# Performance work log

Measured on AMD Instinct MI355X. Metric: run time of the kernel, lower is better.

The kernel has to match this reference:

```python
import jax, jax.numpy as jnp
import numpy as np

N, E = 50000, 800000
IN_DIM, EDGE_DIM, HID, OUT_DIM, L = 128, 16, 64, 8, 4
MSG_EPS = 1e-7  # GENConv eps added to relu(msg)


def layer_norm(x, g, b, eps=1e-5):
    mu = x.mean(-1, keepdims=True)
    var = ((x - mu) ** 2).mean(-1, keepdims=True)
    return (x - mu) * jax.lax.rsqrt(var + eps) * g + b


def segment_softmax(logits, seg, num_segments):
    # numerically stable softmax over edges grouped by destination node
    m = jax.ops.segment_max(logits, seg, num_segments=num_segments)
    m = jnp.where(jnp.isfinite(m), m, 0.0)
    e = jnp.exp(logits - m[seg])
    s = jax.ops.segment_sum(e, seg, num_segments=num_segments)
    return e / (s[seg] + 1e-16)


def gen_conv(x, src, dst, ea, t, W1, b1, g1, be1, W2, b2):
    # GENConv: message = relu(x_j + e_ij) + eps, softmax-aggregate by dst, add root, MLP [h->2h->h]
    msg = jax.nn.relu(x[src] + ea) + MSG_EPS          # [E, H]
    alpha = segment_softmax(msg * t, dst, x.shape[0]) # [E, H]
    agg = jax.ops.segment_sum(msg * alpha, dst, num_segments=x.shape[0])  # [N, H]
    h = agg + x
    h = jax.nn.relu(layer_norm(h @ W1 + b1, g1, be1))  # [N, 2H]
    return h @ W2 + b2                                 # [N, H]


def setup_inputs() -> dict:
    key = jax.random.key(0)
    ks = jax.random.split(key, 16)
    sc = 0.05
    inp = {
        "x": jax.random.normal(ks[0], (N, IN_DIM), jnp.float32),
        "edge_attr": jax.random.normal(ks[1], (E, EDGE_DIM), jnp.float32),
        "node_W": jax.random.normal(ks[2], (IN_DIM, HID), jnp.float32) * sc,
        "node_b": jnp.zeros((HID,), jnp.float32),
        "edge_W": jax.random.normal(ks[3], (EDGE_DIM, HID), jnp.float32) * sc,
        "edge_b": jnp.zeros((HID,), jnp.float32),
        "conv_t": jnp.ones((L,), jnp.float32),
        "conv_W1": jax.random.normal(ks[4], (L, HID, 2 * HID), jnp.float32) * sc,
        "conv_b1": jnp.zeros((L, 2 * HID), jnp.float32),
        "conv_g1": jnp.ones((L, 2 * HID), jnp.float32),
        "conv_be1": jnp.zeros((L, 2 * HID), jnp.float32),
        "conv_W2": jax.random.normal(ks[5], (L, 2 * HID, HID), jnp.float32) * sc,
        "conv_b2": jnp.zeros((L, HID), jnp.float32),
        "ln_g": jnp.ones((L, HID), jnp.float32),
        "ln_b": jnp.zeros((L, HID), jnp.float32),
        "lin_W": jax.random.normal(ks[6], (HID, OUT_DIM), jnp.float32) * sc,
        "lin_b": jnp.zeros((OUT_DIM,), jnp.float32),
        "edge_index": jax.random.randint(ks[7], (2, E), 0, N, jnp.int64),
    }
    return inp


def reference(x, edge_attr, node_W, node_b, edge_W, edge_b,
              conv_t, conv_W1, conv_b1, conv_g1, conv_be1, conv_W2, conv_b2,
              ln_g, ln_b, lin_W, lin_b, edge_index):
    src, dst = edge_index[0], edge_index[1]  # flow: source_to_target
    h = x @ node_W + node_b
    ea = edge_attr @ edge_W + edge_b
    # first layer: conv only (DeeperGCN applies layers[0].conv directly)
    h = gen_conv(h, src, dst, ea, conv_t[0], conv_W1[0], conv_b1[0],
                 conv_g1[0], conv_be1[0], conv_W2[0], conv_b2[0])
    # res+ blocks: x + conv(dropout(relu(norm(x)))); dropout inactive (eval)
    for i in range(1, L):
        z = jax.nn.relu(layer_norm(h, ln_g[i], ln_b[i]))
        h = h + gen_conv(z, src, dst, ea, conv_t[i], conv_W1[i], conv_b1[i],
                         conv_g1[i], conv_be1[i], conv_W2[i], conv_b2[i])
    h = jax.nn.relu(layer_norm(h, ln_g[0], ln_b[0]))
    return h @ lin_W + lin_b
```

## Files before the change

### kernel.cpp

```cpp
#include <hip/hip_runtime.h>
#include <hip/hip_fp16.h>

#define N_NODES 50000
#define N_EDGES 800000
#define IN_DIM  128
#define EDGE_DIM 16
#define HID     64
#define HID2    128
#define OUT_DIM 8
#define N_LAYERS 4
#define NBUCK   391
#define CCHUNK  4096
#define CBLOCKS 196

typedef _Float16 half8 __attribute__((ext_vector_type(8)));
typedef float floatx4 __attribute__((ext_vector_type(4)));

static __device__ __forceinline__ float bcast(float v, int l) {
    return __uint_as_float(__builtin_amdgcn_readlane(__float_as_uint(v), l));
}

__global__ __launch_bounds__(256, 4) void chist_kernel(
    const int* __restrict__ dsts, int* __restrict__ ccnt)
{
    __shared__ int lh[NBUCK];
    for (int i = threadIdx.x; i < NBUCK; i += 256) lh[i] = 0;
    __syncthreads();
    const int base = blockIdx.x * CCHUNK;
#pragma unroll
    for (int i = 0; i < 16; ++i) {
        const int e = base + i * 256 + threadIdx.x;
        if (e < N_EDGES) atomicAdd(&lh[dsts[e] >> 7], 1);
    }
    __syncthreads();
    for (int i = threadIdx.x; i < NBUCK; i += 256)
        if (lh[i]) atomicAdd(&ccnt[i], lh[i]);
}

__global__ __launch_bounds__(256, 1) void cscan_kernel(
    const int* __restrict__ ccnt, int* __restrict__ coff, int* __restrict__ ccur)
{
    __shared__ int part[512];
    const int t = threadIdx.x;
    part[t]       = (t < NBUCK)       ? ccnt[t]       : 0;
    part[t + 256] = (t + 256 < NBUCK) ? ccnt[t + 256] : 0;
    __syncthreads();
    for (int off = 1; off < 512; off <<= 1) {
        const int v0 = (t >= off) ? part[t - off] : 0;
        const int v1 = (t + 256 >= off) ? part[t + 256 - off] : 0;
        __syncthreads();
        part[t] += v0; part[t + 256] += v1;
        __syncthreads();
    }
    if (t < NBUCK) { const int ex = (t > 0) ? part[t - 1] : 0; coff[t] = ex; ccur[t] = ex; }
    const int i2 = t + 256;
    if (i2 < NBUCK) { coff[i2] = part[i2 - 1]; ccur[i2] = part[i2 - 1]; }
    if (t == 0) coff[NBUCK] = part[NBUCK - 1];
}

__global__ __launch_bounds__(256, 4) void cscatter_kernel(
    const int* __restrict__ srcs, const int* __restrict__ dsts,
    int* __restrict__ ccur, uint2* __restrict__ tmp)
{
    __shared__ int lh[NBUCK], lbase[NBUCK], lrank[NBUCK];
    for (int i = threadIdx.x; i < NBUCK; i += 256) { lh[i] = 0; lrank[i] = 0; }
    __syncthreads();
    const int base = blockIdx.x * CCHUNK;
    int myd[16], mys[16];
#pragma unroll
    for (int i = 0; i < 16; ++i) {
        const int e = base + i * 256 + threadIdx.x;
        if (e < N_EDGES) {
            myd[i] = dsts[e]; mys[i] = srcs[e];
            atomicAdd(&lh[myd[i] >> 7], 1);
        } else myd[i] = -1;
    }
    __syncthreads();
    for (int i = threadIdx.x; i < NBUCK; i += 256) {
        const int c = lh[i];
        lbase[i] = c ? atomicAdd(&ccur[i], c) : 0;
    }
    __syncthreads();
#pragma unroll
    for (int i = 0; i < 16; ++i) {
        if (myd[i] >= 0) {
            const int e = base + i * 256 + threadIdx.x;
            const int b = myd[i] >> 7;
            const int r = atomicAdd(&lrank[b], 1);
            tmp[lbase[b] + r] =
                make_uint2((unsigned)mys[i] | ((unsigned)myd[i] << 16),
                           (unsigned)e);
        }
    }
}

__global__ __launch_bounds__(256, 1) void fsort_kernel(
    const uint2* __restrict__ tmp, const int* __restrict__ coff,
    unsigned* __restrict__ sd2, int* __restrict__ eid)
{
    __shared__ uint2 ebuf[4096];
    __shared__ int lh[128], lsc[128];
    const int b = blockIdx.x;
    const int lo = coff[b];
    const int cnt = coff[b + 1] - lo;
    if (threadIdx.x < 128) lh[threadIdx.x] = 0;
    __syncthreads();
    for (int i = threadIdx.x; i < cnt; i += 256) {
        const uint2 v = tmp[lo + i];
        ebuf[i] = v;
        atomicAdd(&lh[(int)(v.x >> 16) - b * 128], 1);
    }
    __syncthreads();
    if (threadIdx.x < 128) lsc[threadIdx.x] = lh[threadIdx.x];
    __syncthreads();
    for (int off = 1; off < 128; off <<= 1) {
        int v = 0;
        if (threadIdx.x < 128 && threadIdx.x >= off) v = lsc[threadIdx.x - off];
        __syncthreads();
        if (threadIdx.x < 128) lsc[threadIdx.x] += v;
        __syncthreads();
    }
    if (threadIdx.x < 128) lh[threadIdx.x] = lsc[threadIdx.x] - lh[threadIdx.x];
    __syncthreads();
    for (int i = threadIdx.x; i < cnt; i += 256) {
        const uint2 v = ebuf[i];
        const int d = (int)(v.x >> 16) - b * 128;
        const int pos = atomicAdd(&lh[d], 1);
        sd2[lo + pos] = v.x;
        eid[lo + pos] = (int)v.y;
    }
}

__global__ __launch_bounds__(256, 2) void node_proj_kernel(
    const float* __restrict__ x, const float* __restrict__ W,
    const float* __restrict__ b, float* __restrict__ h, __half* __restrict__ zh)
{
    __shared__ float xs[4][IN_DIM];
    const int c = threadIdx.x & 63;
    const int local_n = threadIdx.x >> 6;
    float w[IN_DIM];
#pragma unroll
    for (int k = 0; k < IN_DIM; ++k) w[k] = W[k * HID + c];
    const float bias = b[c];

    for (int base = blockIdx.x * 4; base < N_NODES; base += gridDim.x * 4) {
        __syncthreads();
#pragma unroll
        for (int i = 0; i < 2; ++i) {
            int idx = threadIdx.x + i * 256;
            int nn = idx >> 7, kk = idx & 127;
            xs[nn][kk] = x[(base + nn) * IN_DIM + kk];
        }
        __syncthreads();
        const int n = base + local_n;
        float acc = bias;
#pragma unroll
        for (int k4 = 0; k4 < IN_DIM / 4; ++k4) {
            float4 xv = ((const float4*)xs[local_n])[k4];
            acc = fmaf(xv.x, w[k4 * 4 + 0], acc);
            acc = fmaf(xv.y, w[k4 * 4 + 1], acc);
            acc = fmaf(xv.z, w[k4 * 4 + 2], acc);
            acc = fmaf(xv.w, w[k4 * 4 + 3], acc);
        }
        h[n * HID + c] = acc;
        zh[n * HID + c] = __float2half(acc);
    }
}

__global__ __launch_bounds__(256, 4) void edge_emb_kernel(
    const float* __restrict__ ea, const float* __restrict__ W,
    const float* __restrict__ b, const int* __restrict__ eid,
    __half* __restrict__ eah)
{
    __shared__ __half lds_t[4][16 * HID];
    const int lane = threadIdx.x & 63;
    const int waveid = threadIdx.x >> 6;
    const int wave = (blockIdx.x * 256 + threadIdx.x) >> 6;
    const int nwaves = gridDim.x * 4;
    const int m = lane & 15, q = lane >> 4;
    const int NT = N_EDGES / 16;

    half8 bf[4];
#pragma unroll
    for (int blk = 0; blk < 4; ++blk) {
#pragma unroll
        for (int i = 0; i < 8; ++i) {
            const int k = q * 8 + i;
            bf[blk][i] = (k < EDGE_DIM)
                ? (_Float16)W[k * HID + blk * 16 + m] : (_Float16)0.f;
        }
    }
    float bv[4];
#pragma unroll
    for (int blk = 0; blk < 4; ++blk) bv[blk] = b[blk * 16 + m];

    const int ed = lane >> 3, ch = lane & 7;

    for (int tile = wave; tile < NT; tile += nwaves) {
        const int e0 = tile * 16;
        const int eidx = eid[e0 + m];
        half8 af;
#pragma unroll
        for (int i = 0; i < 8; ++i) af[i] = (_Float16)0.f;
        if (q < 2) {
            const float4* ap =
                (const float4*)(ea + (size_t)eidx * EDGE_DIM + q * 8);
            const float4 lo = ap[0];
            const float4 hi = ap[1];
            af[0] = (_Float16)lo.x; af[1] = (_Float16)lo.y;
            af[2] = (_Float16)lo.z; af[3] = (_Float16)lo.w;
            af[4] = (_Float16)hi.x; af[5] = (_Float16)hi.y;
            af[6] = (_Float16)hi.z; af[7] = (_Float16)hi.w;
        }
        floatx4 c[4];
#pragma unroll
        for (int blk = 0; blk < 4; ++blk) {
            floatx4 cin = {bv[blk], bv[blk], bv[blk], bv[blk]};
            c[blk] = __builtin_amdgcn_mfma_f32_16x16x32_f16(
                af, bf[blk], cin, 0, 0, 0);
        }
#pragma unroll
        for (int blk = 0; blk < 4; ++blk)
#pragma unroll
            for (int r = 0; r < 4; ++r)
                lds_t[waveid][(q * 4 + r) * HID + blk * 16 + m] =
                    __float2half(c[blk][r]);
        const float4 v0 =
            *(const float4*)&lds_t[waveid][ed * HID + ch * 8];
        const float4 v1 =
            *(const float4*)&lds_t[waveid][(8 + ed) * HID + ch * 8];
        ((float4*)(eah + (size_t)(e0 + ed) * HID))[ch] = v0;
        ((float4*)(eah + (size_t)(e0 + 8 + ed) * HID))[ch] = v1;
    }
}

__global__ __launch_bounds__(256, 4) void edge_agg_kernel(
    const __half* __restrict__ zh, const __half* __restrict__ eah,
    const unsigned* __restrict__ sd2,
    const float* __restrict__ conv_t, int layer,
    float* __restrict__ p, float* __restrict__ s)
{
    const int lane = threadIdx.x & 63;
    const int wave = (blockIdx.x * 256 + threadIdx.x) >> 6;
    const int nwaves = gridDim.x * 4;
    const float t2 = conv_t[layer] * 1.4426950408889634f;
    const int NT = N_EDGES / 64;

    const _Float16* zf = (const _Float16*)zh;
    const _Float16* ef = (const _Float16*)eah;

    for (int tile = wave; tile < NT; tile += nwaves) {
        const int e0 = tile * 64;
        const unsigned sdv = sd2[e0 + lane];
        const int sv = (int)(sdv & 0xffffu);
        const int dv = (int)(sdv >> 16);
        const int pv = __shfl_up(dv, 1, 64);
        const unsigned long long bmask = __ballot(dv != pv) & ~1ull;
        const _Float16* erow = ef + (size_t)e0 * HID + lane;

        _Float16 za[8], ez[8], zb[8], eb[8];
#pragma unroll
        for (int k = 0; k < 8; ++k) {
            const int a = __builtin_amdgcn_readlane(sv, k);
            za[k] = (zf + (size_t)a * HID)[lane];
            ez[k] = erow[(size_t)k * HID];
        }

        float S = 0.f, P = 0.f;
        int cur = __builtin_amdgcn_readlane(dv, 0);
#pragma unroll
        for (int g = 0; g < 8; ++g) {
            if (g < 7) {
#pragma unroll
                for (int k = 0; k < 8; ++k) {
                    const int a = __builtin_amdgcn_readlane(sv, (g + 1) * 8 + k);
                    zb[k] = (zf + (size_t)a * HID)[lane];
                    eb[k] = erow[(size_t)((g + 1) * 8 + k) * HID];
                }
            }
#pragma unroll
            for (int k = 0; k < 8; ++k) {
                const int j = g * 8 + k;
                if (bmask & (1ull << j)) {
                    unsafeAtomicAdd(&s[(size_t)cur * HID + lane], S);
                    unsafeAtomicAdd(&p[(size_t)cur * HID + lane], P);
                    S = 0.f; P = 0.f;
                    cur = __builtin_amdgcn_readlane(dv, j);
                }
                _Float16 mh = za[k] + ez[k];
                mh = mh > (_Float16)0.f ? mh : (_Float16)0.f;
                const float m = (float)mh + 1e-7f;
                const float xx = __builtin_amdgcn_exp2f(m * t2);
                S += xx;
                P = fmaf(m, xx, P);
            }
            if (g < 7) {
#pragma unroll
                for (int k = 0; k < 8; ++k) { za[k] = zb[k]; ez[k] = eb[k]; }
            }
        }
        unsafeAtomicAdd(&s[(size_t)cur * HID + lane], S);
        unsafeAtomicAdd(&p[(size_t)cur * HID + lane], P);
    }
}

__global__ __launch_bounds__(256, 3) void node_mm1_kernel(
    float* __restrict__ p, float* __restrict__ s,
    const __half* __restrict__ zh,
    const float* __restrict__ W1, const float* __restrict__ b1,
    const float* __restrict__ g1, const float* __restrict__ be1,
    __half* __restrict__ vh)
{
    const int lane = threadIdx.x & 63;
    const int wave = (blockIdx.x * 256 + threadIdx.x) >> 6;
    const int nwaves = gridDim.x * 4;

    float wa[HID], wb[HID];
#pragma unroll
    for (int k = 0; k < HID; ++k) {
        wa[k] = W1[k * HID2 + lane];
        wb[k] = W1[k * HID2 + 64 + lane];
    }
    const float ba = b1[lane],  bb = b1[64 + lane];
    const float ga = g1[lane],  gb = g1[64 + lane];
    const float ca = be1[lane], cb = be1[64 + lane];

    for (int n = wave; n < N_NODES; n += nwaves) {
        const int idx = n * HID + lane;
        const float pv = p[idx];
        const float sv = s[idx];
        const float zv = __half2float(zh[idx]);
        p[idx] = 0.f;
        s[idx] = 0.f;
        const float hv = pv / (sv + 1e-16f) + zv;

        float a0 = 0.f, a1 = 0.f, c0 = 0.f, c1 = 0.f;
#pragma unroll
        for (int k = 0; k < 32; ++k) {
            const float x0 = bcast(hv, k);
            const float x1 = bcast(hv, k + 32);
            a0 = fmaf(x0, wa[k], a0);
            c0 = fmaf(x0, wb[k], c0);
            a1 = fmaf(x1, wa[k + 32], a1);
            c1 = fmaf(x1, wb[k + 32], c1);
        }
        const float ua = (a0 + a1) + ba;
        const float ub = (c0 + c1) + bb;

        float sum = ua + ub;
#pragma unroll
        for (int o = 1; o < 64; o <<= 1) sum += __shfl_xor(sum, o, 64);
        const float mu = sum * (1.f / 128.f);
        const float da = ua - mu, db = ub - mu;
        float q = fmaf(da, da, db * db);
#pragma unroll
        for (int o = 1; o < 64; o <<= 1) q += __shfl_xor(q, o, 64);
        const float rstd = rsqrtf(q * (1.f / 128.f) + 1e-5f);
        const float ya = da * rstd * ga + ca;
        const float yb = db * rstd * gb + cb;
        vh[(size_t)n * HID2 + lane]      = __float2half(ya > 0.f ? ya : 0.f);
        vh[(size_t)n * HID2 + 64 + lane] = __float2half(yb > 0.f ? yb : 0.f);
    }
}

__global__ __launch_bounds__(256, 3) void node_mm2_kernel(
    const __half* __restrict__ vh,
    const float* __restrict__ W2, const float* __restrict__ b2,
    const float* __restrict__ lng, const float* __restrict__ lnb,
    float* __restrict__ h, __half* __restrict__ zh, int residual)
{
    const int lane = threadIdx.x & 63;
    const int wave = (blockIdx.x * 256 + threadIdx.x) >> 6;
    const int nwaves = gridDim.x * 4;

    float wa[HID2 / 2], wb[HID2 / 2];
#pragma unroll
    for (int k = 0; k < HID2 / 2; ++k) {
        wa[k] = W2[k * HID + lane];
        wb[k] = W2[(k + 64) * HID + lane];
    }
    const float bias = b2[lane];
    const float g = lng[lane];
    const float be = lnb[lane];

    for (int n = wave; n < N_NODES; n += nwaves) {
        const float f0 = __half2float(vh[(size_t)n * HID2 + lane]);
        const float f1 = __half2float(vh[(size_t)n * HID2 + 64 + lane]);

        float a0 = 0.f, a1 = 0.f, c0 = 0.f, c1 = 0.f;
#pragma unroll
        for (int k = 0; k < 32; ++k) {
            const float x0 = bcast(f0, k);
            const float x1 = bcast(f0, k + 32);
            const float x2 = bcast(f1, k);
            const float x3 = bcast(f1, k + 32);
            a0 = fmaf(x0, wa[k], a0);
            a1 = fmaf(x1, wa[k + 32], a1);
            c0 = fmaf(x2, wb[k], c0);
            c1 = fmaf(x3, wb[k + 32], c1);
        }
        const float acc = (a0 + a1) + (c0 + c1) + bias;

        const int idx = n * HID + lane;
        const float hn = residual ? (h[idx] + acc) : acc;
        h[idx] = hn;

        float sum = hn;
#pragma unroll
        for (int o = 1; o < 64; o <<= 1) sum += __shfl_xor(sum, o, 64);
        const float mu = sum * (1.f / 64.f);
        const float d = hn - mu;
        float q = d * d;
#pragma unroll
        for (int o = 1; o < 64; o <<= 1) q += __shfl_xor(q, o, 64);
        const float var = q * (1.f / 64.f);
        const float y = d * rsqrtf(var + 1e-5f) * g + be;
        zh[idx] = __float2half(y > 0.f ? y : 0.f);
    }
}

__global__ __launch_bounds__(256, 4) void final_kernel(
    const __half* __restrict__ zh, const float* __restrict__ Wl,
    const float* __restrict__ bl, float* __restrict__ out)
{
    __shared__ float wl[HID * OUT_DIM];
    for (int i = threadIdx.x; i < HID * OUT_DIM; i += 256) wl[i] = Wl[i];
    __syncthreads();
    const int total = N_NODES * OUT_DIM;
    for (int idx = blockIdx.x * 256 + threadIdx.x; idx < total;
         idx += gridDim.x * 256) {
        const int n = idx >> 3, o = idx & 7;
        const __half2* zp = (const __half2*)(zh + (size_t)n * HID);
        float acc = bl[o];
#pragma unroll
        for (int k2 = 0; k2 < HID / 2; ++k2) {
            const float2 f = __half22float2(zp[k2]);
            acc = fmaf(f.x, wl[(k2 * 2 + 0) * OUT_DIM + o], acc);
            acc = fmaf(f.y, wl[(k2 * 2 + 1) * OUT_DIM + o], acc);
        }
        out[idx] = acc;
    }
}

extern "C" void kernel_launch(void* const* d_in, const int* in_sizes, int n_in,
                              void* d_out, int out_size, void* d_ws, size_t ws_size,
                              hipStream_t stream)
{
    const float* x         = (const float*)d_in[0];
    const float* edge_attr = (const float*)d_in[1];
    const float* node_W    = (const float*)d_in[2];
    const float* node_b    = (const float*)d_in[3];
    const float* edge_W    = (const float*)d_in[4];
    const float* edge_b    = (const float*)d_in[5];
    const float* conv_t    = (const float*)d_in[6];
    const float* conv_W1   = (const float*)d_in[7];
    const float* conv_b1   = (const float*)d_in[8];
    const float* conv_g1   = (const float*)d_in[9];
    const float* conv_be1  = (const float*)d_in[10];
    const float* conv_W2   = (const float*)d_in[11];
    const float* conv_b2   = (const float*)d_in[12];
    const float* ln_g      = (const float*)d_in[13];
    const float* ln_b      = (const float*)d_in[14];
    const float* lin_W     = (const float*)d_in[15];
    const float* lin_b     = (const float*)d_in[16];
    const int*   edge_index= (const int*)d_in[17];
    const int*   srcs = edge_index;
    const int*   dsts = edge_index + N_EDGES;
    float* out = (float*)d_out;

    float* h   = (float*)d_ws;
    float* p   = h   + N_NODES * HID;
    float* s   = p   + N_NODES * HID;
    __half* vh  = (__half*)(s + N_NODES * HID);
    __half* zh  = vh + (size_t)N_NODES * HID2;
    __half* eah = zh + (size_t)N_NODES * HID;
    uint2* tmp  = (uint2*)(eah + (size_t)N_EDGES * HID);
    unsigned* sd2 = (unsigned*)(tmp + N_EDGES);
    int* eid    = (int*)(sd2 + N_EDGES);
    int* ccnt   = eid + N_EDGES;
    int* coff   = ccnt + NBUCK;
    int* ccur   = coff + NBUCK + 1;

    hipMemsetAsync(ccnt, 0, (size_t)NBUCK * sizeof(int), stream);
    chist_kernel<<<CBLOCKS, 256, 0, stream>>>(dsts, ccnt);
    cscan_kernel<<<1, 256, 0, stream>>>(ccnt, coff, ccur);
    cscatter_kernel<<<CBLOCKS, 256, 0, stream>>>(srcs, dsts, ccur, tmp);
    fsort_kernel<<<NBUCK, 256, 0, stream>>>(tmp, coff, sd2, eid);

    node_proj_kernel<<<2048, 256, 0, stream>>>(x, node_W, node_b, h, zh);
    edge_emb_kernel<<<3125, 256, 0, stream>>>(edge_attr, edge_W, edge_b, eid, eah);

    hipMemsetAsync(p, 0, (size_t)2 * N_NODES * HID * sizeof(float), stream);

    for (int layer = 0; layer < N_LAYERS; ++layer) {
        edge_agg_kernel<<<3125, 256, 0, stream>>>(zh, eah, sd2,
                                                  conv_t, layer, p, s);
        node_mm1_kernel<<<2048, 256, 0, stream>>>(
            p, s, zh,
            conv_W1 + (size_t)layer * HID * HID2, conv_b1 + layer * HID2,
            conv_g1 + layer * HID2, conv_be1 + layer * HID2, vh);
        const float* gz = (layer < N_LAYERS - 1) ? (ln_g + (layer + 1) * HID) : ln_g;
        const float* bz = (layer < N_LAYERS - 1) ? (ln_b + (layer + 1) * HID) : ln_b;
        node_mm2_kernel<<<2048, 256, 0, stream>>>(
            vh, conv_W2 + (size_t)layer * HID2 * HID, conv_b2 + layer * HID,
            gz, bz, h, zh, layer > 0 ? 1 : 0);
    }
    final_kernel<<<1024, 256, 0, stream>>>(zh, lin_W, lin_b, out);
}
```

Before: 670.4 us.

## Fuse edge embedding projection into per-layer edge aggregation kernel

Removes the precomputed fp16 edge-embedding buffer and instead recomputes the edge_attr projection with MFMA inside each layer's aggregation kernel, staging results through a rotated LDS buffer for per-lane access. This trades reading a large materialised edge-feature array four times for gathering the smaller raw edge attributes and doing redundant matrix work per layer. It raises LDS usage and register pressure and may reduce occupancy.

```diff
diff --git a/kernel.cpp b/kernel.cpp
--- a/kernel.cpp
+++ b/kernel.cpp
@@ -14,6 +14,7 @@
 #define CBLOCKS 196
 
 typedef _Float16 half8 __attribute__((ext_vector_type(8)));
+typedef _Float16 half2f __attribute__((ext_vector_type(2)));
 typedef float floatx4 __attribute__((ext_vector_type(4)));
 
 static __device__ __forceinline__ float bcast(float v, int l) {
@@ -167,18 +168,23 @@
     }
 }
 
-__global__ __launch_bounds__(256, 4) void edge_emb_kernel(
-    const float* __restrict__ ea, const float* __restrict__ W,
-    const float* __restrict__ b, const int* __restrict__ eid,
-    __half* __restrict__ eah)
-{
-    __shared__ __half lds_t[4][16 * HID];
+__global__ __launch_bounds__(256, 4) void edge_agg_kernel(
+    const __half* __restrict__ zh,
+    const float* __restrict__ ea, const float* __restrict__ eW,
+    const float* __restrict__ eb_, const int* __restrict__ eid,
+    const unsigned* __restrict__ sd2,
+    const float* __restrict__ conv_t, int layer,
+    float* __restrict__ p, float* __restrict__ s)
+{
+    __shared__ _Float16 lbuf[4][64 * 64];
     const int lane = threadIdx.x & 63;
     const int waveid = threadIdx.x >> 6;
     const int wave = (blockIdx.x * 256 + threadIdx.x) >> 6;
     const int nwaves = gridDim.x * 4;
+    const float t2 = conv_t[layer] * 1.4426950408889634f;
+    const int NT = N_EDGES / 64;
     const int m = lane & 15, q = lane >> 4;
-    const int NT = N_EDGES / 16;
+    const int rot = m * 4;
 
     half8 bf[4];
 #pragma unroll
@@ -187,67 +193,15 @@
         for (int i = 0; i < 8; ++i) {
             const int k = q * 8 + i;
             bf[blk][i] = (k < EDGE_DIM)
-                ? (_Float16)W[k * HID + blk * 16 + m] : (_Float16)0.f;
+                ? (_Float16)eW[k * HID + blk * 16 + m] : (_Float16)0.f;
         }
     }
     float bv[4];
 #pragma unroll
-    for (int blk = 0; blk < 4; ++blk) bv[blk] = b[blk * 16 + m];
-
-    const int ed = lane >> 3, ch = lane & 7;
-
-    for (int tile = wave; tile < NT; tile += nwaves) {
-        const int e0 = tile * 16;
-        const int eidx = eid[e0 + m];
-        half8 af;
-#pragma unroll
-        for (int i = 0; i < 8; ++i) af[i] = (_Float16)0.f;
-        if (q < 2) {
-            const float4* ap =
-                (const float4*)(ea + (size_t)eidx * EDGE_DIM + q * 8);
-            const float4 lo = ap[0];
-            const float4 hi = ap[1];
-            af[0] = (_Float16)lo.x; af[1] = (_Float16)lo.y;
-            af[2] = (_Float16)lo.z; af[3] = (_Float16)lo.w;
-            af[4] = (_Float16)hi.x; af[5] = (_Float16)hi.y;
-            af[6] = (_Float16)hi.z; af[7] = (_Float16)hi.w;
-        }
-        floatx4 c[4];
-#pragma unroll
-        for (int blk = 0; blk < 4; ++blk) {
-            floatx4 cin = {bv[blk], bv[blk], bv[blk], bv[blk]};
-            c[blk] = __builtin_amdgcn_mfma_f32_16x16x32_f16(
-                af, bf[blk], cin, 0, 0, 0);
-        }
-#pragma unroll
-        for (int blk = 0; blk < 4; ++blk)
-#pragma unroll
-            for (int r = 0; r < 4; ++r)
-                lds_t[waveid][(q * 4 + r) * HID + blk * 16 + m] =
-                    __float2half(c[blk][r]);
-        const float4 v0 =
-            *(const float4*)&lds_t[waveid][ed * HID + ch * 8];
-        const float4 v1 =
-            *(const float4*)&lds_t[waveid][(8 + ed) * HID + ch * 8];
-        ((float4*)(eah + (size_t)(e0 + ed) * HID))[ch] = v0;
-        ((float4*)(eah + (size_t)(e0 + 8 + ed) * HID))[ch] = v1;
-    }
-}
-
-__global__ __launch_bounds__(256, 4) void edge_agg_kernel(
-    const __half* __restrict__ zh, const __half* __restrict__ eah,
-    const unsigned* __restrict__ sd2,
-    const float* __restrict__ conv_t, int layer,
-    float* __restrict__ p, float* __restrict__ s)
-{
-    const int lane = threadIdx.x & 63;
-    const int wave = (blockIdx.x * 256 + threadIdx.x) >> 6;
-    const int nwaves = gridDim.x * 4;
-    const float t2 = conv_t[layer] * 1.4426950408889634f;
-    const int NT = N_EDGES / 64;
+    for (int blk = 0; blk < 4; ++blk) bv[blk] = eb_[blk * 16 + m];
 
     const _Float16* zf = (const _Float16*)zh;
-    const _Float16* ef = (const _Float16*)eah;
+    _Float16* lrow = &lbuf[waveid][lane * 64];
 
     for (int tile = wave; tile < NT; tile += nwaves) {
         const int e0 = tile * 64;
@@ -256,14 +210,52 @@
         const int dv = (int)(sdv >> 16);
         const int pv = __shfl_up(dv, 1, 64);
         const unsigned long long bmask = __ballot(dv != pv) & ~1ull;
-        const _Float16* erow = ef + (size_t)e0 * HID + lane;
+
+        half8 afv[4];
+#pragma unroll
+        for (int t = 0; t < 4; ++t) {
+            const int eidx = eid[e0 + t * 16 + m];
+#pragma unroll
+            for (int i = 0; i < 8; ++i) afv[t][i] = (_Float16)0.f;
+            if (q < 2) {
+                const float4* ap =
+                    (const float4*)(ea + (size_t)eidx * EDGE_DIM + q * 8);
+                const float4 lo = ap[0];
+                const float4 hi = ap[1];
+                afv[t][0] = (_Float16)lo.x; afv[t][1] = (_Float16)lo.y;
+                afv[t][2] = (_Float16)lo.z; afv[t][3] = (_Float16)lo.w;
+                afv[t][4] = (_Float16)hi.x; afv[t][5] = (_Float16)hi.y;
+                afv[t][6] = (_Float16)hi.z; afv[t][7] = (_Float16)hi.w;
+            }
+        }
+#pragma unroll
+        for (int t = 0; t < 4; ++t) {
+#pragma unroll
+            for (int blk = 0; blk < 4; ++blk) {
+                floatx4 cin = {bv[blk], bv[blk], bv[blk], bv[blk]};
+                const floatx4 cc = __builtin_amdgcn_mfma_f32_16x16x32_f16(
+                    afv[t], bf[blk], cin, 0, 0, 0);
+                const int feat = blk * 16 + m;
+                const int col = (t * 16 + q * 4 + rot) & 63;
+                half2f h01, h23;
+                h01[0] = (_Float16)cc[0]; h01[1] = (_Float16)cc[1];
+                h23[0] = (_Float16)cc[2]; h23[1] = (_Float16)cc[3];
+                *(half2f*)&lbuf[waveid][feat * 64 + col]     = h01;
+                *(half2f*)&lbuf[waveid][feat * 64 + col + 2] = h23;
+            }
+        }
 
         _Float16 za[8], ez[8], zb[8], eb[8];
 #pragma unroll
         for (int k = 0; k < 8; ++k) {
             const int a = __builtin_amdgcn_readlane(sv, k);
             za[k] = (zf + (size_t)a * HID)[lane];
-            ez[k] = erow[(size_t)k * HID];
+        }
+#pragma unroll
+        for (int k2 = 0; k2 < 4; ++k2) {
+            const int col = (k2 * 2 + rot) & 63;
+            const half2f v = *(const half2f*)&lrow[col];
+            ez[2 * k2] = v[0]; ez[2 * k2 + 1] = v[1];
         }
 
         float S = 0.f, P = 0.f;
@@ -275,7 +267,12 @@
                 for (int k = 0; k < 8; ++k) {
                     const int a = __builtin_amdgcn_readlane(sv, (g + 1) * 8 + k);
                     zb[k] = (zf + (size_t)a * HID)[lane];
-                    eb[k] = erow[(size_t)((g + 1) * 8 + k) * HID];
+                }
+#pragma unroll
+                for (int k2 = 0; k2 < 4; ++k2) {
+                    const int col = ((g + 1) * 8 + k2 * 2 + rot) & 63;
+                    const half2f v = *(const half2f*)&lrow[col];
+                    eb[2 * k2] = v[0]; eb[2 * k2 + 1] = v[1];
                 }
             }
 #pragma unroll
@@ -289,10 +286,10 @@
                 }
                 _Float16 mh = za[k] + ez[k];
                 mh = mh > (_Float16)0.f ? mh : (_Float16)0.f;
-                const float m = (float)mh + 1e-7f;
-                const float xx = __builtin_amdgcn_exp2f(m * t2);
+                const float mm = (float)mh + 1e-7f;
+                const float xx = __builtin_amdgcn_exp2f(mm * t2);
                 S += xx;
-                P = fmaf(m, xx, P);
+                P = fmaf(mm, xx, P);
             }
             if (g < 7) {
 #pragma unroll
@@ -473,8 +470,7 @@
     float* s   = p   + N_NODES * HID;
     __half* vh  = (__half*)(s + N_NODES * HID);
     __half* zh  = vh + (size_t)N_NODES * HID2;
-    __half* eah = zh + (size_t)N_NODES * HID;
-    uint2* tmp  = (uint2*)(eah + (size_t)N_EDGES * HID);
+    uint2* tmp  = (uint2*)(zh + (size_t)N_NODES * HID);
     unsigned* sd2 = (unsigned*)(tmp + N_EDGES);
     int* eid    = (int*)(sd2 + N_EDGES);
     int* ccnt   = eid + N_EDGES;
@@ -488,13 +484,12 @@
     fsort_kernel<<<NBUCK, 256, 0, stream>>>(tmp, coff, sd2, eid);
 
     node_proj_kernel<<<2048, 256, 0, stream>>>(x, node_W, node_b, h, zh);
-    edge_emb_kernel<<<3125, 256, 0, stream>>>(edge_attr, edge_W, edge_b, eid, eah);
 
     hipMemsetAsync(p, 0, (size_t)2 * N_NODES * HID * sizeof(float), stream);
 
     for (int layer = 0; layer < N_LAYERS; ++layer) {
-        edge_agg_kernel<<<3125, 256, 0, stream>>>(zh, eah, sd2,
-                                                  conv_t, layer, p, s);
+        edge_agg_kernel<<<3125, 256, 0, stream>>>(
+            zh, edge_attr, edge_W, edge_b, eid, sd2, conv_t, layer, p, s);
         node_mm1_kernel<<<2048, 256, 0, stream>>>(
             p, s, zh,
             conv_W1 + (size_t)layer * HID * HID2, conv_b1 + layer * HID2,
```

After: 748.4 us. 11.6% more time.

## Switch edge aggregation to CSR per-node waves, removing atomics and memsets

Applied to the files above, without the earlier changes.

The sort kernel now also writes per-node row offsets (CSR) over the dst-sorted edge list. Edge aggregation assigns one wave per destination node and walks its incoming edges with a 4-deep prefetch. It writes P and S directly instead of using atomic adds, which also removes the zero-fill memset and the clearing stores in node_mm1. The risk is load imbalance from variable node degree (about 16 on average), which leaves many partially used 64-edge batches and shorter memory-level parallelism per wave than the old 64-edge tiles.

```diff
diff --git a/kernel.cpp b/kernel.cpp
--- a/kernel.cpp
+++ b/kernel.cpp
@@ -96,7 +96,8 @@
 
 __global__ __launch_bounds__(256, 1) void fsort_kernel(
     const uint2* __restrict__ tmp, const int* __restrict__ coff,
-    unsigned* __restrict__ sd2, int* __restrict__ eid)
+    unsigned* __restrict__ sd2, int* __restrict__ eid,
+    int* __restrict__ roff)
 {
     __shared__ uint2 ebuf[4096];
     __shared__ int lh[128], lsc[128];
@@ -120,7 +121,12 @@
         if (threadIdx.x < 128) lsc[threadIdx.x] += v;
         __syncthreads();
     }
-    if (threadIdx.x < 128) lh[threadIdx.x] = lsc[threadIdx.x] - lh[threadIdx.x];
+    if (threadIdx.x < 128) {
+        lh[threadIdx.x] = lsc[threadIdx.x] - lh[threadIdx.x];
+        roff[b * 128 + threadIdx.x] = lo + lh[threadIdx.x];
+        if (b == NBUCK - 1 && threadIdx.x == 127)
+            roff[NBUCK * 128] = lo + cnt;
+    }
     __syncthreads();
     for (int i = threadIdx.x; i < cnt; i += 256) {
         const uint2 v = ebuf[i];
@@ -236,7 +242,7 @@
 
 __global__ __launch_bounds__(256, 4) void edge_agg_kernel(
     const __half* __restrict__ zh, const __half* __restrict__ eah,
-    const unsigned* __restrict__ sd2,
+    const unsigned* __restrict__ sd2, const int* __restrict__ roff,
     const float* __restrict__ conv_t, int layer,
     float* __restrict__ p, float* __restrict__ s)
 {
@@ -244,68 +250,67 @@
     const int wave = (blockIdx.x * 256 + threadIdx.x) >> 6;
     const int nwaves = gridDim.x * 4;
     const float t2 = conv_t[layer] * 1.4426950408889634f;
-    const int NT = N_EDGES / 64;
+    const float et2 = 1e-7f * t2;
 
     const _Float16* zf = (const _Float16*)zh;
     const _Float16* ef = (const _Float16*)eah;
 
-    for (int tile = wave; tile < NT; tile += nwaves) {
-        const int e0 = tile * 64;
-        const unsigned sdv = sd2[e0 + lane];
-        const int sv = (int)(sdv & 0xffffu);
-        const int dv = (int)(sdv >> 16);
-        const int pv = __shfl_up(dv, 1, 64);
-        const unsigned long long bmask = __ballot(dv != pv) & ~1ull;
-        const _Float16* erow = ef + (size_t)e0 * HID + lane;
-
-        _Float16 za[8], ez[8], zb[8], eb[8];
-#pragma unroll
-        for (int k = 0; k < 8; ++k) {
-            const int a = __builtin_amdgcn_readlane(sv, k);
-            za[k] = (zf + (size_t)a * HID)[lane];
-            ez[k] = erow[(size_t)k * HID];
-        }
-
+    for (int n = wave; n < N_NODES; n += nwaves) {
+        const int lo = roff[n];
+        const int d = roff[n + 1] - lo;
         float S = 0.f, P = 0.f;
-        int cur = __builtin_amdgcn_readlane(dv, 0);
-#pragma unroll
-        for (int g = 0; g < 8; ++g) {
-            if (g < 7) {
-#pragma unroll
-                for (int k = 0; k < 8; ++k) {
-                    const int a = __builtin_amdgcn_readlane(sv, (g + 1) * 8 + k);
-                    zb[k] = (zf + (size_t)a * HID)[lane];
-                    eb[k] = erow[(size_t)((g + 1) * 8 + k) * HID];
+
+        for (int base = 0; base < d; base += 64) {
+            const int cnt = (d - base < 64) ? (d - base) : 64;
+            const unsigned sdv = sd2[lo + base + (lane < cnt ? lane : cnt - 1)];
+            const _Float16* ep = ef + (size_t)(lo + base) * HID + lane;
+
+            _Float16 zr[4], er[4];
+#pragma unroll
+            for (int k = 0; k < 4; ++k) {
+                if (k < cnt) {
+                    const int a = (int)(__builtin_amdgcn_readlane(sdv, k) & 0xffffu);
+                    zr[k] = zf[(size_t)a * HID + lane];
+                    er[k] = ep[(size_t)k * HID];
                 }
             }
-#pragma unroll
-            for (int k = 0; k < 8; ++k) {
-                const int j = g * 8 + k;
-                if (bmask & (1ull << j)) {
-                    unsafeAtomicAdd(&s[(size_t)cur * HID + lane], S);
-                    unsafeAtomicAdd(&p[(size_t)cur * HID + lane], P);
-                    S = 0.f; P = 0.f;
-                    cur = __builtin_amdgcn_readlane(dv, j);
+            int i = 0;
+            for (; i + 4 <= cnt; i += 4) {
+#pragma unroll
+                for (int k = 0; k < 4; ++k) {
+                    _Float16 mh = zr[k] + er[k];
+                    mh = mh > (_Float16)0.f ? mh : (_Float16)0.f;
+                    const float mm = (float)mh;
+                    const float xx = __builtin_amdgcn_exp2f(fmaf(mm, t2, et2));
+                    S += xx;
+                    P = fmaf(mm + 1e-7f, xx, P);
+                    const int nx = i + 4 + k;
+                    if (nx < cnt) {
+                        const int a = (int)(__builtin_amdgcn_readlane(sdv, nx) & 0xffffu);
+                        zr[k] = zf[(size_t)a * HID + lane];
+                        er[k] = ep[(size_t)nx * HID];
+                    }
                 }
-                _Float16 mh = za[k] + ez[k];
-                mh = mh > (_Float16)0.f ? mh : (_Float16)0.f;
-                const float m = (float)mh + 1e-7f;
-                const float xx = __builtin_amdgcn_exp2f(m * t2);
-                S += xx;
-                P = fmaf(m, xx, P);
             }
-            if (g < 7) {
-#pragma unroll
-                for (int k = 0; k < 8; ++k) { za[k] = zb[k]; ez[k] = eb[k]; }
+#pragma unroll
+            for (int k = 0; k < 4; ++k) {
+                if (i + k < cnt) {
+                    _Float16 mh = zr[k] + er[k];
+                    mh = mh > (_Float16)0.f ? mh : (_Float16)0.f;
+                    const float mm = (float)mh;
+                    const float xx = __builtin_amdgcn_exp2f(fmaf(mm, t2, et2));
+                    S += xx;
+                    P = fmaf(mm + 1e-7f, xx, P);
+                }
             }
         }
-        unsafeAtomicAdd(&s[(size_t)cur * HID + lane], S);
-        unsafeAtomicAdd(&p[(size_t)cur * HID + lane], P);
+        p[(size_t)n * HID + lane] = P;
+        s[(size_t)n * HID + lane] = S;
     }
 }
 
 __global__ __launch_bounds__(256, 3) void node_mm1_kernel(
-    float* __restrict__ p, float* __restrict__ s,
+    const float* __restrict__ p, const float* __restrict__ s,
     const __half* __restrict__ zh,
     const float* __restrict__ W1, const float* __restrict__ b1,
     const float* __restrict__ g1, const float* __restrict__ be1,
@@ -330,8 +335,6 @@
         const float pv = p[idx];
         const float sv = s[idx];
         const float zv = __half2float(zh[idx]);
-        p[idx] = 0.f;
-        s[idx] = 0.f;
         const float hv = pv / (sv + 1e-16f) + zv;
 
         float a0 = 0.f, a1 = 0.f, c0 = 0.f, c1 = 0.f;
@@ -477,7 +480,8 @@
     uint2* tmp  = (uint2*)(eah + (size_t)N_EDGES * HID);
     unsigned* sd2 = (unsigned*)(tmp + N_EDGES);
     int* eid    = (int*)(sd2 + N_EDGES);
-    int* ccnt   = eid + N_EDGES;
+    int* roff   = eid + N_EDGES;
+    int* ccnt   = roff + NBUCK * 128 + 1;
     int* coff   = ccnt + NBUCK;
     int* ccur   = coff + NBUCK + 1;
 
@@ -485,15 +489,13 @@
     chist_kernel<<<CBLOCKS, 256, 0, stream>>>(dsts, ccnt);
     cscan_kernel<<<1, 256, 0, stream>>>(ccnt, coff, ccur);
     cscatter_kernel<<<CBLOCKS, 256, 0, stream>>>(srcs, dsts, ccur, tmp);
-    fsort_kernel<<<NBUCK, 256, 0, stream>>>(tmp, coff, sd2, eid);
+    fsort_kernel<<<NBUCK, 256, 0, stream>>>(tmp, coff, sd2, eid, roff);
 
     node_proj_kernel<<<2048, 256, 0, stream>>>(x, node_W, node_b, h, zh);
     edge_emb_kernel<<<3125, 256, 0, stream>>>(edge_attr, edge_W, edge_b, eid, eah);
 
-    hipMemsetAsync(p, 0, (size_t)2 * N_NODES * HID * sizeof(float), stream);
-
     for (int layer = 0; layer < N_LAYERS; ++layer) {
-        edge_agg_kernel<<<3125, 256, 0, stream>>>(zh, eah, sd2,
+        edge_agg_kernel<<<6250, 256, 0, stream>>>(zh, eah, sd2, roff,
                                                   conv_t, layer, p, s);
         node_mm1_kernel<<<2048, 256, 0, stream>>>(
             p, s, zh,
```

After: 781.8 us. 16.6% more time.

## Fuse node MLP kernels and deepen edge aggregation prefetch

Applied to the files above, without the earlier changes.

Merges the two node MLP kernels into one that splits each node's 128-wide hidden layer across two waves and combines partial results through shared memory. This removes the intermediate fp16 hidden buffer and one launch per layer. The edge aggregation kernel now loads all 64 edge embeddings up front and gathers source features 16 at a time, with occupancy lowered to 3 blocks per SM to fit the extra registers. The fused kernel adds block-level barriers per node pair.

```diff
diff --git a/kernel.cpp b/kernel.cpp
--- a/kernel.cpp
+++ b/kernel.cpp
@@ -234,7 +234,7 @@
     }
 }
 
-__global__ __launch_bounds__(256, 4) void edge_agg_kernel(
+__global__ __launch_bounds__(256, 3) void edge_agg_kernel(
     const __half* __restrict__ zh, const __half* __restrict__ eah,
     const unsigned* __restrict__ sd2,
     const float* __restrict__ conv_t, int layer,
@@ -252,51 +252,54 @@
     for (int tile = wave; tile < NT; tile += nwaves) {
         const int e0 = tile * 64;
         const unsigned sdv = sd2[e0 + lane];
+        const _Float16* erow = ef + (size_t)e0 * HID + lane;
+
+        _Float16 ez[64];
+#pragma unroll
+        for (int k = 0; k < 64; ++k) ez[k] = erow[(size_t)k * HID];
+
         const int sv = (int)(sdv & 0xffffu);
         const int dv = (int)(sdv >> 16);
         const int pv = __shfl_up(dv, 1, 64);
         const unsigned long long bmask = __ballot(dv != pv) & ~1ull;
-        const _Float16* erow = ef + (size_t)e0 * HID + lane;
-
-        _Float16 za[8], ez[8], zb[8], eb[8];
-#pragma unroll
-        for (int k = 0; k < 8; ++k) {
+
+        _Float16 za[16], zb[16];
+#pragma unroll
+        for (int k = 0; k < 16; ++k) {
             const int a = __builtin_amdgcn_readlane(sv, k);
-            za[k] = (zf + (size_t)a * HID)[lane];
-            ez[k] = erow[(size_t)k * HID];
+            za[k] = zf[(size_t)a * HID + lane];
         }
 
         float S = 0.f, P = 0.f;
         int cur = __builtin_amdgcn_readlane(dv, 0);
 #pragma unroll
-        for (int g = 0; g < 8; ++g) {
-            if (g < 7) {
-#pragma unroll
-                for (int k = 0; k < 8; ++k) {
-                    const int a = __builtin_amdgcn_readlane(sv, (g + 1) * 8 + k);
-                    zb[k] = (zf + (size_t)a * HID)[lane];
-                    eb[k] = erow[(size_t)((g + 1) * 8 + k) * HID];
+        for (int g = 0; g < 4; ++g) {
+            if (g < 3) {
+#pragma unroll
+                for (int k = 0; k < 16; ++k) {
+                    const int a = __builtin_amdgcn_readlane(sv, (g + 1) * 16 + k);
+                    zb[k] = zf[(size_t)a * HID + lane];
                 }
             }
 #pragma unroll
-            for (int k = 0; k < 8; ++k) {
-                const int j = g * 8 + k;
+            for (int k = 0; k < 16; ++k) {
+                const int j = g * 16 + k;
                 if (bmask & (1ull << j)) {
                     unsafeAtomicAdd(&s[(size_t)cur * HID + lane], S);
                     unsafeAtomicAdd(&p[(size_t)cur * HID + lane], P);
                     S = 0.f; P = 0.f;
                     cur = __builtin_amdgcn_readlane(dv, j);
                 }
-                _Float16 mh = za[k] + ez[k];
+                _Float16 mh = za[k] + ez[j];
                 mh = mh > (_Float16)0.f ? mh : (_Float16)0.f;
-                const float m = (float)mh + 1e-7f;
-                const float xx = __builtin_amdgcn_exp2f(m * t2);
+                const float mm = (float)mh + 1e-7f;
+                const float xx = __builtin_amdgcn_exp2f(mm * t2);
                 S += xx;
-                P = fmaf(m, xx, P);
+                P = fmaf(mm, xx, P);
             }
-            if (g < 7) {
-#pragma unroll
-                for (int k = 0; k < 8; ++k) { za[k] = zb[k]; ez[k] = eb[k]; }
+            if (g < 3) {
+#pragma unroll
+                for (int k = 0; k < 16; ++k) za[k] = zb[k];
             }
         }
         unsafeAtomicAdd(&s[(size_t)cur * HID + lane], S);
@@ -304,118 +307,88 @@
     }
 }
 
-__global__ __launch_bounds__(256, 3) void node_mm1_kernel(
+__global__ __launch_bounds__(256, 3) void node_mlp_kernel(
     float* __restrict__ p, float* __restrict__ s,
-    const __half* __restrict__ zh,
     const float* __restrict__ W1, const float* __restrict__ b1,
     const float* __restrict__ g1, const float* __restrict__ be1,
-    __half* __restrict__ vh)
-{
+    const float* __restrict__ W2, const float* __restrict__ b2,
+    const float* __restrict__ lng, const float* __restrict__ lnb,
+    float* __restrict__ h, __half* zh, int residual)
+{
+    __shared__ float part1[2][HID];
+    __shared__ float red[2][2][2];
     const int lane = threadIdx.x & 63;
-    const int wave = (blockIdx.x * 256 + threadIdx.x) >> 6;
-    const int nwaves = gridDim.x * 4;
-
-    float wa[HID], wb[HID];
-#pragma unroll
-    for (int k = 0; k < HID; ++k) {
-        wa[k] = W1[k * HID2 + lane];
-        wb[k] = W1[k * HID2 + 64 + lane];
-    }
-    const float ba = b1[lane],  bb = b1[64 + lane];
-    const float ga = g1[lane],  gb = g1[64 + lane];
-    const float ca = be1[lane], cb = be1[64 + lane];
-
-    for (int n = wave; n < N_NODES; n += nwaves) {
+    const int waveid = threadIdx.x >> 6;
+    const int nodesel = waveid >> 1;
+    const int w = waveid & 1;
+    const int j = w * HID + lane;
+
+    float w1c[HID], w2c[HID];
+#pragma unroll
+    for (int k = 0; k < HID; ++k) w1c[k] = W1[k * HID2 + j];
+#pragma unroll
+    for (int k = 0; k < HID; ++k) w2c[k] = W2[(w * HID + k) * HID + lane];
+    const float b1j = b1[j], g1j = g1[j], be1j = be1[j];
+    const float b2c = b2[lane], gz = lng[lane], bz = lnb[lane];
+
+    for (int base = blockIdx.x * 2; base < N_NODES; base += gridDim.x * 2) {
+        const int n = base + nodesel;
         const int idx = n * HID + lane;
         const float pv = p[idx];
         const float sv = s[idx];
-        const float zv = __half2float(zh[idx]);
-        p[idx] = 0.f;
-        s[idx] = 0.f;
-        const float hv = pv / (sv + 1e-16f) + zv;
-
-        float a0 = 0.f, a1 = 0.f, c0 = 0.f, c1 = 0.f;
+        const float hv = pv / (sv + 1e-16f) + __half2float(zh[idx]);
+
+        float a0 = 0.f, a1 = 0.f;
 #pragma unroll
         for (int k = 0; k < 32; ++k) {
-            const float x0 = bcast(hv, k);
-            const float x1 = bcast(hv, k + 32);
-            a0 = fmaf(x0, wa[k], a0);
-            c0 = fmaf(x0, wb[k], c0);
-            a1 = fmaf(x1, wa[k + 32], a1);
-            c1 = fmaf(x1, wb[k + 32], c1);
-        }
-        const float ua = (a0 + a1) + ba;
-        const float ub = (c0 + c1) + bb;
-
-        float sum = ua + ub;
-#pragma unroll
-        for (int o = 1; o < 64; o <<= 1) sum += __shfl_xor(sum, o, 64);
-        const float mu = sum * (1.f / 128.f);
-        const float da = ua - mu, db = ub - mu;
-        float q = fmaf(da, da, db * db);
-#pragma unroll
-        for (int o = 1; o < 64; o <<= 1) q += __shfl_xor(q, o, 64);
-        const float rstd = rsqrtf(q * (1.f / 128.f) + 1e-5f);
-        const float ya = da * rstd * ga + ca;
-        const float yb = db * rstd * gb + cb;
-        vh[(size_t)n * HID2 + lane]      = __float2half(ya > 0.f ? ya : 0.f);
-        vh[(size_t)n * HID2 + 64 + lane] = __float2half(yb > 0.f ? yb : 0.f);
-    }
-}
-
-__global__ __launch_bounds__(256, 3) void node_mm2_kernel(
-    const __half* __restrict__ vh,
-    const float* __restrict__ W2, const float* __restrict__ b2,
-    const float* __restrict__ lng, const float* __restrict__ lnb,
-    float* __restrict__ h, __half* __restrict__ zh, int residual)
-{
-    const int lane = threadIdx.x & 63;
-    const int wave = (blockIdx.x * 256 + threadIdx.x) >> 6;
-    const int nwaves = gridDim.x * 4;
-
-    float wa[HID2 / 2], wb[HID2 / 2];
-#pragma unroll
-    for (int k = 0; k < HID2 / 2; ++k) {
-        wa[k] = W2[k * HID + lane];
-        wb[k] = W2[(k + 64) * HID + lane];
-    }
-    const float bias = b2[lane];
-    const float g = lng[lane];
-    const float be = lnb[lane];
-
-    for (int n = wave; n < N_NODES; n += nwaves) {
-        const float f0 = __half2float(vh[(size_t)n * HID2 + lane]);
-        const float f1 = __half2float(vh[(size_t)n * HID2 + 64 + lane]);
-
-        float a0 = 0.f, a1 = 0.f, c0 = 0.f, c1 = 0.f;
+            a0 = fmaf(bcast(hv, k),      w1c[k],      a0);
+            a1 = fmaf(bcast(hv, k + 32), w1c[k + 32], a1);
+        }
+        const float u = (a0 + a1) + b1j;
+
+        float su = u;
+#pragma unroll
+        for (int o = 1; o < 64; o <<= 1) su += __shfl_xor(su, o, 64);
+        if (lane == 0) red[nodesel][0][w] = su;
+        __syncthreads();
+        const float mu = (red[nodesel][0][0] + red[nodesel][0][1]) * (1.f / 128.f);
+        if (w == 0) { p[idx] = 0.f; s[idx] = 0.f; }
+
+        const float d = u - mu;
+        float qd = d * d;
+#pragma unroll
+        for (int o = 1; o < 64; o <<= 1) qd += __shfl_xor(qd, o, 64);
+        if (lane == 0) red[nodesel][1][w] = qd;
+        __syncthreads();
+        const float var = (red[nodesel][1][0] + red[nodesel][1][1]) * (1.f / 128.f);
+        const float y = d * rsqrtf(var + 1e-5f) * g1j + be1j;
+        const float v = y > 0.f ? y : 0.f;
+
+        float q0 = 0.f, q1 = 0.f;
 #pragma unroll
         for (int k = 0; k < 32; ++k) {
-            const float x0 = bcast(f0, k);
-            const float x1 = bcast(f0, k + 32);
-            const float x2 = bcast(f1, k);
-            const float x3 = bcast(f1, k + 32);
-            a0 = fmaf(x0, wa[k], a0);
-            a1 = fmaf(x1, wa[k + 32], a1);
-            c0 = fmaf(x2, wb[k], c0);
-            c1 = fmaf(x3, wb[k + 32], c1);
-        }
-        const float acc = (a0 + a1) + (c0 + c1) + bias;
-
-        const int idx = n * HID + lane;
-        const float hn = residual ? (h[idx] + acc) : acc;
-        h[idx] = hn;
-
-        float sum = hn;
-#pragma unroll
-        for (int o = 1; o < 64; o <<= 1) sum += __shfl_xor(sum, o, 64);
-        const float mu = sum * (1.f / 64.f);
-        const float d = hn - mu;
-        float q = d * d;
-#pragma unroll
-        for (int o = 1; o < 64; o <<= 1) q += __shfl_xor(q, o, 64);
-        const float var = q * (1.f / 64.f);
-        const float y = d * rsqrtf(var + 1e-5f) * g + be;
-        zh[idx] = __float2half(y > 0.f ? y : 0.f);
+            q0 = fmaf(bcast(v, k),      w2c[k],      q0);
+            q1 = fmaf(bcast(v, k + 32), w2c[k + 32], q1);
+        }
+        const float partial = q0 + q1;
+        if (w == 1) part1[nodesel][lane] = partial;
+        __syncthreads();
+        if (w == 0) {
+            const float acc = partial + part1[nodesel][lane] + b2c;
+            const float hn = residual ? (h[idx] + acc) : acc;
+            h[idx] = hn;
+            float s2 = hn;
+#pragma unroll
+            for (int o = 1; o < 64; o <<= 1) s2 += __shfl_xor(s2, o, 64);
+            const float mu2 = s2 * (1.f / 64.f);
+            const float d2 = hn - mu2;
+            float q2 = d2 * d2;
+#pragma unroll
+            for (int o = 1; o < 64; o <<= 1) q2 += __shfl_xor(q2, o, 64);
+            const float var2 = q2 * (1.f / 64.f);
+            const float yy = d2 * rsqrtf(var2 + 1e-5f) * gz + bz;
+            zh[idx] = __float2half(yy > 0.f ? yy : 0.f);
+        }
     }
 }
 
@@ -471,8 +444,7 @@
     float* h   = (float*)d_ws;
     float* p   = h   + N_NODES * HID;
     float* s   = p   + N_NODES * HID;
-    __half* vh  = (__half*)(s + N_NODES * HID);
-    __half* zh  = vh + (size_t)N_NODES * HID2;
+    __half* zh  = (__half*)(s + N_NODES * HID);
     __half* eah = zh + (size_t)N_NODES * HID;
     uint2* tmp  = (uint2*)(eah + (size_t)N_EDGES * HID);
     unsigned* sd2 = (unsigned*)(tmp + N_EDGES);
@@ -495,14 +467,13 @@
     for (int layer = 0; layer < N_LAYERS; ++layer) {
         edge_agg_kernel<<<3125, 256, 0, stream>>>(zh, eah, sd2,
                                                   conv_t, layer, p, s);
-        node_mm1_kernel<<<2048, 256, 0, stream>>>(
-            p, s, zh,
-            conv_W1 + (size_t)layer * HID * HID2, conv_b1 + layer * HID2,
-            conv_g1 + layer * HID2, conv_be1 + layer * HID2, vh);
         const float* gz = (layer < N_LAYERS - 1) ? (ln_g + (layer + 1) * HID) : ln_g;
         const float* bz = (layer < N_LAYERS - 1) ? (ln_b + (layer + 1) * HID) : ln_b;
-        node_mm2_kernel<<<2048, 256, 0, stream>>>(
-            vh, conv_W2 + (size_t)layer * HID2 * HID, conv_b2 + layer * HID,
+        node_mlp_kernel<<<2048, 256, 0, stream>>>(
+            p, s,
+            conv_W1 + (size_t)layer * HID * HID2, conv_b1 + layer * HID2,
+            conv_g1 + layer * HID2, conv_be1 + layer * HID2,
+            conv_W2 + (size_t)layer * HID2 * HID, conv_b2 + layer * HID,
             gz, bz, h, zh, layer > 0 ? 1 : 0);
     }
     final_kernel<<<1024, 256, 0, stream>>>(zh, lin_W, lin_b, out);
```

Result: slower. 769.0 us (+14.7%).
